# Performance work log

Hardware: AMD Instinct MI355X
Metric: run time of the kernel (lower is better)

## Reference

```python
import jax, jax.numpy as jnp
import numpy as np

B, T, NG, NH, DH = 16, 1024, 4, 1, 768
NS = 2  # states: (h, c)


def _lstm_layer(states0, Wx, R, b):
    """Fused LSTM scan for one layer.

    states0: [NS, B, NH, DH] initial (h, c)
    Wx:      [B, T, NG, NH, DH] precomputed input projections
    R:       [NG, NH, DH, DH] recurrent weights
    b:       [NG, NH, DH] biases
    returns: hs [T, NS, B, NH, DH] stacked (h, c) per step
    """
    h0, c0 = states0[0], states0[1]
    bb = b[:, None]  # [NG, 1, NH, DH] -> broadcasts over batch

    def step(carry, wx_t):
        h, c = carry  # [B, NH, DH]
        # gates: [NG, B, NH, DH]
        gates = wx_t + jnp.einsum('bhd,ghde->gbhe', h, R) + bb
        i = jax.nn.sigmoid(gates[0])
        f = jax.nn.sigmoid(gates[1])
        z = jnp.tanh(gates[2])
        o = jax.nn.sigmoid(gates[3])
        c_new = f * c + i * z
        h_new = o * jnp.tanh(c_new)
        return (h_new, c_new), jnp.stack([h_new, c_new])

    wx_tfirst = jnp.transpose(Wx, (1, 2, 0, 3, 4))  # [T, NG, B, NH, DH]
    _, hs = jax.lax.scan(step, (h0, c0), wx_tfirst)
    return hs  # [T, NS, B, NH, DH]


def setup_inputs() -> dict:
    key = jax.random.key(0)
    ks = jax.random.split(key, 6)
    s = 0.02
    return {
        'states': jnp.zeros((1, NS, B, NH, DH), jnp.float32),
        'Wx0': jax.random.normal(ks[0], (B, T, NG, NH, DH), jnp.float32) * s,
        'R0': jax.random.normal(ks[1], (NG, NH, DH, DH), jnp.float32) * s,
        'b0': jax.random.normal(ks[2], (NG, NH, DH), jnp.float32) * s,
        'Wx1': jax.random.normal(ks[3], (B, T, NG, NH, DH), jnp.float32) * s,
        'R1': jax.random.normal(ks[4], (NG, NH, DH, DH), jnp.float32) * s,
        'b1': jax.random.normal(ks[5], (NG, NH, DH), jnp.float32) * s,
    }


def reference(states, Wx0, R0, b0, Wx1, R1, b1):
    out = states  # [1, NS, B, NH, DH]
    h = None
    last_h = None
    for Wx, R, b in ((Wx0, R0, b0), (Wx1, R1, b1)):
        hs = _lstm_layer(out[0], Wx, R, b)  # [T, NS, B, NH, DH]
        h = hs
        last_h = hs[-1:]  # [1, NS, B, NH, DH]
        out = last_h  # last state of this layer is initial state of next
    return (h, last_h, out)
```

## Files before the change

kernel.cpp:

```cpp
#include <hip/hip_runtime.h>
#include <math.h>

#define NWG    48
#define TT     1024
#define BSZ    16
#define DHH    768
#define NGG    4
#define EC     16
#define LDR    776
#define GP     17
#define KS     192
#define FSTR   32

typedef __attribute__((ext_vector_type(8))) short bf16x8_t;
typedef __attribute__((ext_vector_type(4))) float f32x4_t;

__device__ __forceinline__ unsigned short f2bf(float f) {
  union { float f; unsigned int u; } v; v.f = f;
  return (unsigned short)((v.u + 0x7fffu + ((v.u >> 16) & 1u)) >> 16);
}

__device__ __forceinline__ bf16x8_t ld_h_frag(const unsigned short* p) {
  union { bf16x8_t v; unsigned long long q[2]; } u;
  u.q[0] = __hip_atomic_load((const unsigned long long*)p,       __ATOMIC_RELAXED, __HIP_MEMORY_SCOPE_AGENT);
  u.q[1] = __hip_atomic_load((const unsigned long long*)(p + 4), __ATOMIC_RELAXED, __HIP_MEMORY_SCOPE_AGENT);
  return u.v;
}

__global__ void lstm_init_ws(int* flags) {
  for (int i = threadIdx.x; i < NWG * FSTR; i += blockDim.x) flags[i] = 0;
}

__device__ __forceinline__ void grid_barrier(int* flags, int wg, int epoch, int lane, int wv) {
  __syncthreads();
  if (wv == 0) {
    if (lane == 0)
      __hip_atomic_store(flags + wg * FSTR, epoch, __ATOMIC_RELAXED, __HIP_MEMORY_SCOPE_AGENT);
    for (;;) {
      int v = (lane < NWG)
            ? __hip_atomic_load(flags + lane * FSTR, __ATOMIC_RELAXED, __HIP_MEMORY_SCOPE_AGENT)
            : epoch;
      if (__all(v >= epoch)) break;
      __builtin_amdgcn_s_sleep(1);
    }
  }
  __syncthreads();
}

__global__ __launch_bounds__(256, 1) void lstm_persistent(
    const float* __restrict__ states,
    const float* __restrict__ Wx0, const float* __restrict__ R0, const float* __restrict__ b0,
    const float* __restrict__ Wx1, const float* __restrict__ R1, const float* __restrict__ b1,
    float* __restrict__ out, int* __restrict__ flags, unsigned short* __restrict__ hbuf)
{
  extern __shared__ unsigned char smem[];
  unsigned short* r_lds    = (unsigned short*)smem;
  float*          part_lds = (float*)(r_lds + NGG * EC * LDR);
  float*          b_lds    = part_lds + 4 * NGG * BSZ * GP;

  const int tid  = threadIdx.x;
  const int lane = tid & 63;
  const int wv   = tid >> 6;
  const int bb   = tid >> 4;
  const int el   = tid & 15;
  const int wg   = blockIdx.x;
  const int e0   = wg * EC;
  const int m    = lane & 15;
  const int q    = lane >> 4;

  float creg = states[(BSZ + bb) * DHH + e0 + el];
  {
    unsigned hv = f2bf(states[bb * DHH + e0 + el]);
    unsigned pv = (unsigned)__shfl_xor((int)hv, 1, 64);
    if ((el & 1) == 0)
      __hip_atomic_store((unsigned*)(hbuf + bb * DHH + e0 + el), hv | (pv << 16),
                         __ATOMIC_RELAXED, __HIP_MEMORY_SCOPE_AGENT);
  }

  int epoch = 1;
  grid_barrier(flags, wg, epoch, lane, wv);

  for (int layer = 0; layer < 2; ++layer) {
    const float* Wx = layer ? Wx1 : Wx0;
    const float* Rm = layer ? R1  : R0;
    const float* bv = layer ? b1  : b0;

    for (int i = tid; i < NGG * DHH; i += 256) {
      const int g = i / DHH, d = i - g * DHH;
      const float* src = Rm + (g * DHH + d) * DHH + e0;
      #pragma unroll
      for (int n = 0; n < EC; ++n)
        r_lds[(g * EC + n) * LDR + d] = f2bf(src[n]);
    }
    if (tid < NGG * EC) b_lds[tid] = bv[(tid >> 4) * DHH + e0 + (tid & 15)];
    __syncthreads();

    for (int t = 0; t < TT; ++t) {
      const int gs = layer * TT + t;
      const unsigned short* __restrict__ hsrc = hbuf + (gs & 1) * (BSZ * DHH);
      unsigned short* __restrict__ hdst = hbuf + ((gs + 1) & 1) * (BSZ * DHH);

      const float* wxp = Wx + ((bb * TT + t) * NGG) * DHH + e0 + el;
      const float wxv0 = wxp[0];
      const float wxv1 = wxp[DHH];
      const float wxv2 = wxp[2 * DHH];
      const float wxv3 = wxp[3 * DHH];

      {
        const unsigned short* ha = hsrc + m * DHH + wv * KS + q * 8;
        const unsigned short* rb = r_lds + m * LDR + wv * KS + q * 8;
        f32x4_t ac0 = {0.f, 0.f, 0.f, 0.f};
        f32x4_t ac1 = ac0, ac2 = ac0, ac3 = ac0;
        #pragma unroll
        for (int kk = 0; kk < KS; kk += 32) {
          bf16x8_t av = ld_h_frag(ha + kk);
          ac0 = __builtin_amdgcn_mfma_f32_16x16x32_bf16(av, *(const bf16x8_t*)(rb + kk),               ac0, 0, 0, 0);
          ac1 = __builtin_amdgcn_mfma_f32_16x16x32_bf16(av, *(const bf16x8_t*)(rb + EC * LDR + kk),    ac1, 0, 0, 0);
          ac2 = __builtin_amdgcn_mfma_f32_16x16x32_bf16(av, *(const bf16x8_t*)(rb + 2 * EC * LDR + kk), ac2, 0, 0, 0);
          ac3 = __builtin_amdgcn_mfma_f32_16x16x32_bf16(av, *(const bf16x8_t*)(rb + 3 * EC * LDR + kk), ac3, 0, 0, 0);
        }
        #pragma unroll
        for (int r = 0; r < 4; ++r) {
          part_lds[((wv * NGG + 0) * BSZ + q * 4 + r) * GP + m] = ac0[r];
          part_lds[((wv * NGG + 1) * BSZ + q * 4 + r) * GP + m] = ac1[r];
          part_lds[((wv * NGG + 2) * BSZ + q * 4 + r) * GP + m] = ac2[r];
          part_lds[((wv * NGG + 3) * BSZ + q * 4 + r) * GP + m] = ac3[r];
        }
      }
      __syncthreads();

      {
        float gi = wxv0 + b_lds[0 * EC + el];
        float gf = wxv1 + b_lds[1 * EC + el];
        float gz = wxv2 + b_lds[2 * EC + el];
        float go = wxv3 + b_lds[3 * EC + el];
        #pragma unroll
        for (int w = 0; w < 4; ++w) {
          gi += part_lds[((w * NGG + 0) * BSZ + bb) * GP + el];
          gf += part_lds[((w * NGG + 1) * BSZ + bb) * GP + el];
          gz += part_lds[((w * NGG + 2) * BSZ + bb) * GP + el];
          go += part_lds[((w * NGG + 3) * BSZ + bb) * GP + el];
        }
        const float iv = 1.f / (1.f + __expf(-gi));
        const float fv = 1.f / (1.f + __expf(-gf));
        const float zv = tanhf(gz);
        const float ov = 1.f / (1.f + __expf(-go));
        const float cnew = fv * creg + iv * zv;
        const float hnew = ov * tanhf(cnew);
        creg = cnew;

        unsigned hv = f2bf(hnew);
        unsigned pv = (unsigned)__shfl_xor((int)hv, 1, 64);
        if ((el & 1) == 0)
          __hip_atomic_store((unsigned*)(hdst + bb * DHH + e0 + el), hv | (pv << 16),
                             __ATOMIC_RELAXED, __HIP_MEMORY_SCOPE_AGENT);

        if (layer == 1) {
          out[((t * 2 + 0) * BSZ + bb) * DHH + e0 + el] = hnew;
          out[((t * 2 + 1) * BSZ + bb) * DHH + e0 + el] = cnew;
          if (t == TT - 1) {
            const int HS = TT * 2 * BSZ * DHH;
            out[HS + (0 * BSZ + bb) * DHH + e0 + el] = hnew;
            out[HS + (1 * BSZ + bb) * DHH + e0 + el] = cnew;
            out[HS + 2 * BSZ * DHH + (0 * BSZ + bb) * DHH + e0 + el] = hnew;
            out[HS + 2 * BSZ * DHH + (1 * BSZ + bb) * DHH + e0 + el] = cnew;
          }
        }
      }

      if (gs != 2 * TT - 1) {
        ++epoch;
        grid_barrier(flags, wg, epoch, lane, wv);
      }
    }
  }
}

extern "C" void kernel_launch(void* const* d_in, const int* in_sizes, int n_in,
                              void* d_out, int out_size, void* d_ws, size_t ws_size,
                              hipStream_t stream) {
  const float* states = (const float*)d_in[0];
  const float* Wx0    = (const float*)d_in[1];
  const float* R0     = (const float*)d_in[2];
  const float* b0     = (const float*)d_in[3];
  const float* Wx1    = (const float*)d_in[4];
  const float* R1     = (const float*)d_in[5];
  const float* b1     = (const float*)d_in[6];
  float* out = (float*)d_out;

  int* flags = (int*)d_ws;
  unsigned short* hbuf = (unsigned short*)((char*)d_ws + 8192);

  const int smem_bytes = (NGG * EC * LDR) * 2 +
                         (4 * NGG * BSZ * GP + NGG * EC) * 4;

  static bool attr_set = false;
  if (!attr_set) {
    hipFuncSetAttribute((const void*)lstm_persistent,
                        hipFuncAttributeMaxDynamicSharedMemorySize, smem_bytes);
    attr_set = true;
  }

  lstm_init_ws<<<dim3(1), dim3(256), 0, stream>>>(flags);
  lstm_persistent<<<dim3(NWG), dim3(256), smem_bytes, stream>>>(
      states, Wx0, R0, b0, Wx1, R1, b1, out, flags, hbuf);
}
```

Baseline: 7.959 ms.

## Keep recurrent weights in registers, prefetch Wx, and make all waves poll the grid barrier

Recurrent weight fragments are loaded once per layer from LDS into registers, so the per-step MFMA loop no longer reads LDS. The next step's Wx values are prefetched one step ahead, and the h fragments are fetched with raw sc1 global loads issued together before a single wait. The grid barrier changes so that every wave polls the flags without sleeping, which removes one __syncthreads and the s_sleep delay. Sigmoid and tanh now use exp-based approximations and the biases live in registers. In exchange the kernel uses much more register space and relies on hand-written inline asm for memory ordering.

```diff
diff --git a/kernel.cpp b/kernel.cpp
--- a/kernel.cpp
+++ b/kernel.cpp
@@ -15,36 +15,44 @@
 typedef __attribute__((ext_vector_type(8))) short bf16x8_t;
 typedef __attribute__((ext_vector_type(4))) float f32x4_t;
 
+#define MF(a,b,c) __builtin_amdgcn_mfma_f32_16x16x32_bf16((a),(b),(c),0,0,0)
+
 __device__ __forceinline__ unsigned short f2bf(float f) {
   union { float f; unsigned int u; } v; v.f = f;
   return (unsigned short)((v.u + 0x7fffu + ((v.u >> 16) & 1u)) >> 16);
 }
-
-__device__ __forceinline__ bf16x8_t ld_h_frag(const unsigned short* p) {
-  union { bf16x8_t v; unsigned long long q[2]; } u;
-  u.q[0] = __hip_atomic_load((const unsigned long long*)p,       __ATOMIC_RELAXED, __HIP_MEMORY_SCOPE_AGENT);
-  u.q[1] = __hip_atomic_load((const unsigned long long*)(p + 4), __ATOMIC_RELAXED, __HIP_MEMORY_SCOPE_AGENT);
-  return u.v;
+__device__ __forceinline__ float sigm(float x)      { return 1.f / (1.f + __expf(-x)); }
+__device__ __forceinline__ float tanh_fast(float x) { return 1.f - 2.f / (__expf(2.f * x) + 1.f); }
+
+__device__ __forceinline__ void ldg_a16_sc(bf16x8_t& d, const unsigned short* p) {
+  asm volatile("global_load_dwordx4 %0, %1, off sc1" : "=v"(d) : "v"(p));
+}
+__device__ __forceinline__ void ldg_f32(float& d, const float* p) {
+  asm volatile("global_load_dword %0, %1, off" : "=v"(d) : "v"(p));
+}
+__device__ __forceinline__ void stg_u32_sc(unsigned* p, unsigned v) {
+  asm volatile("global_store_dword %0, %1, off sc1" :: "v"(p), "v"(v) : "memory");
+}
+__device__ __forceinline__ void wait_vm0() {
+  asm volatile("s_waitcnt vmcnt(0)" ::: "memory");
+}
+__device__ __forceinline__ void wait_lgkm_barrier() {
+  asm volatile("s_waitcnt lgkmcnt(0)\ns_barrier" ::: "memory");
+}
+__device__ __forceinline__ void wait_vm0_barrier() {
+  asm volatile("s_waitcnt vmcnt(0) lgkmcnt(0)\ns_barrier" ::: "memory");
 }
 
 __global__ void lstm_init_ws(int* flags) {
   for (int i = threadIdx.x; i < NWG * FSTR; i += blockDim.x) flags[i] = 0;
 }
 
-__device__ __forceinline__ void grid_barrier(int* flags, int wg, int epoch, int lane, int wv) {
-  __syncthreads();
-  if (wv == 0) {
-    if (lane == 0)
-      __hip_atomic_store(flags + wg * FSTR, epoch, __ATOMIC_RELAXED, __HIP_MEMORY_SCOPE_AGENT);
-    for (;;) {
-      int v = (lane < NWG)
-            ? __hip_atomic_load(flags + lane * FSTR, __ATOMIC_RELAXED, __HIP_MEMORY_SCOPE_AGENT)
-            : epoch;
-      if (__all(v >= epoch)) break;
-      __builtin_amdgcn_s_sleep(1);
-    }
-  }
-  __syncthreads();
+__device__ __forceinline__ void poll_flags(const int* fp, bool self_or_oob, int epoch) {
+  for (;;) {
+    int v = self_or_oob ? epoch
+                        : __hip_atomic_load(fp, __ATOMIC_RELAXED, __HIP_MEMORY_SCOPE_AGENT);
+    if (__all(v >= epoch)) break;
+  }
 }
 
 __global__ __launch_bounds__(256, 1) void lstm_persistent(
@@ -56,7 +64,6 @@
   extern __shared__ unsigned char smem[];
   unsigned short* r_lds    = (unsigned short*)smem;
   float*          part_lds = (float*)(r_lds + NGG * EC * LDR);
-  float*          b_lds    = part_lds + 4 * NGG * BSZ * GP;
 
   const int tid  = threadIdx.x;
   const int lane = tid & 63;
@@ -68,17 +75,33 @@
   const int m    = lane & 15;
   const int q    = lane >> 4;
 
+  const int aofs = m * DHH + wv * KS + q * 8;
+  const int hofs = bb * DHH + e0 + el;
+  const int* fp  = flags + (lane < NWG ? lane : 0) * FSTR;
+  const bool self_skip = (lane >= NWG) || (lane == wg);
+
   float creg = states[(BSZ + bb) * DHH + e0 + el];
   {
     unsigned hv = f2bf(states[bb * DHH + e0 + el]);
     unsigned pv = (unsigned)__shfl_xor((int)hv, 1, 64);
     if ((el & 1) == 0)
-      __hip_atomic_store((unsigned*)(hbuf + bb * DHH + e0 + el), hv | (pv << 16),
-                         __ATOMIC_RELAXED, __HIP_MEMORY_SCOPE_AGENT);
+      stg_u32_sc((unsigned*)(hbuf + hofs), hv | (pv << 16));
   }
 
   int epoch = 1;
-  grid_barrier(flags, wg, epoch, lane, wv);
+  wait_vm0_barrier();
+  if (tid == 0)
+    __hip_atomic_store(flags + wg * FSTR, epoch, __ATOMIC_RELAXED, __HIP_MEMORY_SCOPE_AGENT);
+  float pw0, pw1, pw2, pw3;
+  {
+    const float* wxp = Wx0 + ((bb * TT + 0) * NGG) * DHH + e0 + el;
+    ldg_f32(pw0, wxp); ldg_f32(pw1, wxp + DHH);
+    ldg_f32(pw2, wxp + 2 * DHH); ldg_f32(pw3, wxp + 3 * DHH);
+  }
+  poll_flags(fp, self_skip, epoch);
+  __builtin_amdgcn_sched_barrier(0);
+
+  int oofs = bb * DHH + e0 + el;
 
   for (int layer = 0; layer < 2; ++layer) {
     const float* Wx = layer ? Wx1 : Wx0;
@@ -92,48 +115,72 @@
       for (int n = 0; n < EC; ++n)
         r_lds[(g * EC + n) * LDR + d] = f2bf(src[n]);
     }
-    if (tid < NGG * EC) b_lds[tid] = bv[(tid >> 4) * DHH + e0 + (tid & 15)];
     __syncthreads();
+
+    bf16x8_t B00,B01,B02,B03,B04,B05, B10,B11,B12,B13,B14,B15,
+             B20,B21,B22,B23,B24,B25, B30,B31,B32,B33,B34,B35;
+    {
+      const unsigned short* rb = r_lds + m * LDR + wv * KS + q * 8;
+      B00 = *(const bf16x8_t*)(rb + 0*EC*LDR +   0); B01 = *(const bf16x8_t*)(rb + 0*EC*LDR +  32);
+      B02 = *(const bf16x8_t*)(rb + 0*EC*LDR +  64); B03 = *(const bf16x8_t*)(rb + 0*EC*LDR +  96);
+      B04 = *(const bf16x8_t*)(rb + 0*EC*LDR + 128); B05 = *(const bf16x8_t*)(rb + 0*EC*LDR + 160);
+      B10 = *(const bf16x8_t*)(rb + 1*EC*LDR +   0); B11 = *(const bf16x8_t*)(rb + 1*EC*LDR +  32);
+      B12 = *(const bf16x8_t*)(rb + 1*EC*LDR +  64); B13 = *(const bf16x8_t*)(rb + 1*EC*LDR +  96);
+      B14 = *(const bf16x8_t*)(rb + 1*EC*LDR + 128); B15 = *(const bf16x8_t*)(rb + 1*EC*LDR + 160);
+      B20 = *(const bf16x8_t*)(rb + 2*EC*LDR +   0); B21 = *(const bf16x8_t*)(rb + 2*EC*LDR +  32);
+      B22 = *(const bf16x8_t*)(rb + 2*EC*LDR +  64); B23 = *(const bf16x8_t*)(rb + 2*EC*LDR +  96);
+      B24 = *(const bf16x8_t*)(rb + 2*EC*LDR + 128); B25 = *(const bf16x8_t*)(rb + 2*EC*LDR + 160);
+      B30 = *(const bf16x8_t*)(rb + 3*EC*LDR +   0); B31 = *(const bf16x8_t*)(rb + 3*EC*LDR +  32);
+      B32 = *(const bf16x8_t*)(rb + 3*EC*LDR +  64); B33 = *(const bf16x8_t*)(rb + 3*EC*LDR +  96);
+      B34 = *(const bf16x8_t*)(rb + 3*EC*LDR + 128); B35 = *(const bf16x8_t*)(rb + 3*EC*LDR + 160);
+    }
+    const float bi_ = bv[0 * DHH + e0 + el];
+    const float bf_ = bv[1 * DHH + e0 + el];
+    const float bz_ = bv[2 * DHH + e0 + el];
+    const float bo_ = bv[3 * DHH + e0 + el];
 
     for (int t = 0; t < TT; ++t) {
       const int gs = layer * TT + t;
       const unsigned short* __restrict__ hsrc = hbuf + (gs & 1) * (BSZ * DHH);
       unsigned short* __restrict__ hdst = hbuf + ((gs + 1) & 1) * (BSZ * DHH);
 
-      const float* wxp = Wx + ((bb * TT + t) * NGG) * DHH + e0 + el;
-      const float wxv0 = wxp[0];
-      const float wxv1 = wxp[DHH];
-      const float wxv2 = wxp[2 * DHH];
-      const float wxv3 = wxp[3 * DHH];
-
+      const float qw0 = pw0, qw1 = pw1, qw2 = pw2, qw3 = pw3;
+
+      bf16x8_t av0, av1, av2, av3, av4, av5;
       {
-        const unsigned short* ha = hsrc + m * DHH + wv * KS + q * 8;
-        const unsigned short* rb = r_lds + m * LDR + wv * KS + q * 8;
-        f32x4_t ac0 = {0.f, 0.f, 0.f, 0.f};
-        f32x4_t ac1 = ac0, ac2 = ac0, ac3 = ac0;
-        #pragma unroll
-        for (int kk = 0; kk < KS; kk += 32) {
-          bf16x8_t av = ld_h_frag(ha + kk);
-          ac0 = __builtin_amdgcn_mfma_f32_16x16x32_bf16(av, *(const bf16x8_t*)(rb + kk),               ac0, 0, 0, 0);
-          ac1 = __builtin_amdgcn_mfma_f32_16x16x32_bf16(av, *(const bf16x8_t*)(rb + EC * LDR + kk),    ac1, 0, 0, 0);
-          ac2 = __builtin_amdgcn_mfma_f32_16x16x32_bf16(av, *(const bf16x8_t*)(rb + 2 * EC * LDR + kk), ac2, 0, 0, 0);
-          ac3 = __builtin_amdgcn_mfma_f32_16x16x32_bf16(av, *(const bf16x8_t*)(rb + 3 * EC * LDR + kk), ac3, 0, 0, 0);
-        }
-        #pragma unroll
-        for (int r = 0; r < 4; ++r) {
-          part_lds[((wv * NGG + 0) * BSZ + q * 4 + r) * GP + m] = ac0[r];
-          part_lds[((wv * NGG + 1) * BSZ + q * 4 + r) * GP + m] = ac1[r];
-          part_lds[((wv * NGG + 2) * BSZ + q * 4 + r) * GP + m] = ac2[r];
-          part_lds[((wv * NGG + 3) * BSZ + q * 4 + r) * GP + m] = ac3[r];
-        }
-      }
-      __syncthreads();
+        const unsigned short* ha = hsrc + aofs;
+        ldg_a16_sc(av0, ha +   0); ldg_a16_sc(av1, ha +  32);
+        ldg_a16_sc(av2, ha +  64); ldg_a16_sc(av3, ha +  96);
+        ldg_a16_sc(av4, ha + 128); ldg_a16_sc(av5, ha + 160);
+      }
+      if (gs + 1 < 2 * TT) {
+        const int g2 = gs + 1, l2 = g2 >> 10, t2 = g2 & (TT - 1);
+        const float* wxp = (l2 ? Wx1 : Wx0) + ((bb * TT + t2) * NGG) * DHH + e0 + el;
+        ldg_f32(pw0, wxp); ldg_f32(pw1, wxp + DHH);
+        ldg_f32(pw2, wxp + 2 * DHH); ldg_f32(pw3, wxp + 3 * DHH);
+      }
+      wait_vm0();
+      __builtin_amdgcn_sched_barrier(0);
+
+      f32x4_t ac0 = {0.f,0.f,0.f,0.f}, ac1 = ac0, ac2 = ac0, ac3 = ac0;
+      ac0 = MF(av0,B00,ac0); ac1 = MF(av0,B10,ac1); ac2 = MF(av0,B20,ac2); ac3 = MF(av0,B30,ac3);
+      ac0 = MF(av1,B01,ac0); ac1 = MF(av1,B11,ac1); ac2 = MF(av1,B21,ac2); ac3 = MF(av1,B31,ac3);
+      ac0 = MF(av2,B02,ac0); ac1 = MF(av2,B12,ac1); ac2 = MF(av2,B22,ac2); ac3 = MF(av2,B32,ac3);
+      ac0 = MF(av3,B03,ac0); ac1 = MF(av3,B13,ac1); ac2 = MF(av3,B23,ac2); ac3 = MF(av3,B33,ac3);
+      ac0 = MF(av4,B04,ac0); ac1 = MF(av4,B14,ac1); ac2 = MF(av4,B24,ac2); ac3 = MF(av4,B34,ac3);
+      ac0 = MF(av5,B05,ac0); ac1 = MF(av5,B15,ac1); ac2 = MF(av5,B25,ac2); ac3 = MF(av5,B35,ac3);
+
+      #pragma unroll
+      for (int r = 0; r < 4; ++r) {
+        part_lds[((wv * NGG + 0) * BSZ + q * 4 + r) * GP + m] = ac0[r];
+        part_lds[((wv * NGG + 1) * BSZ + q * 4 + r) * GP + m] = ac1[r];
+        part_lds[((wv * NGG + 2) * BSZ + q * 4 + r) * GP + m] = ac2[r];
+        part_lds[((wv * NGG + 3) * BSZ + q * 4 + r) * GP + m] = ac3[r];
+      }
+      wait_lgkm_barrier();
 
       {
-        float gi = wxv0 + b_lds[0 * EC + el];
-        float gf = wxv1 + b_lds[1 * EC + el];
-        float gz = wxv2 + b_lds[2 * EC + el];
-        float go = wxv3 + b_lds[3 * EC + el];
+        float gi = qw0 + bi_, gf = qw1 + bf_, gz = qw2 + bz_, go = qw3 + bo_;
         #pragma unroll
         for (int w = 0; w < 4; ++w) {
           gi += part_lds[((w * NGG + 0) * BSZ + bb) * GP + el];
@@ -141,36 +188,37 @@
           gz += part_lds[((w * NGG + 2) * BSZ + bb) * GP + el];
           go += part_lds[((w * NGG + 3) * BSZ + bb) * GP + el];
         }
-        const float iv = 1.f / (1.f + __expf(-gi));
-        const float fv = 1.f / (1.f + __expf(-gf));
-        const float zv = tanhf(gz);
-        const float ov = 1.f / (1.f + __expf(-go));
+        const float iv = sigm(gi), fv = sigm(gf), zv = tanh_fast(gz), ov = sigm(go);
         const float cnew = fv * creg + iv * zv;
-        const float hnew = ov * tanhf(cnew);
+        const float hnew = ov * tanh_fast(cnew);
         creg = cnew;
 
         unsigned hv = f2bf(hnew);
         unsigned pv = (unsigned)__shfl_xor((int)hv, 1, 64);
         if ((el & 1) == 0)
-          __hip_atomic_store((unsigned*)(hdst + bb * DHH + e0 + el), hv | (pv << 16),
-                             __ATOMIC_RELAXED, __HIP_MEMORY_SCOPE_AGENT);
+          stg_u32_sc((unsigned*)(hdst + hofs), hv | (pv << 16));
 
         if (layer == 1) {
-          out[((t * 2 + 0) * BSZ + bb) * DHH + e0 + el] = hnew;
-          out[((t * 2 + 1) * BSZ + bb) * DHH + e0 + el] = cnew;
+          out[oofs] = hnew;
+          out[oofs + BSZ * DHH] = cnew;
           if (t == TT - 1) {
             const int HS = TT * 2 * BSZ * DHH;
-            out[HS + (0 * BSZ + bb) * DHH + e0 + el] = hnew;
-            out[HS + (1 * BSZ + bb) * DHH + e0 + el] = cnew;
-            out[HS + 2 * BSZ * DHH + (0 * BSZ + bb) * DHH + e0 + el] = hnew;
-            out[HS + 2 * BSZ * DHH + (1 * BSZ + bb) * DHH + e0 + el] = cnew;
+            out[HS + bb * DHH + e0 + el] = hnew;
+            out[HS + BSZ * DHH + bb * DHH + e0 + el] = cnew;
+            out[HS + 2 * BSZ * DHH + bb * DHH + e0 + el] = hnew;
+            out[HS + 3 * BSZ * DHH + bb * DHH + e0 + el] = cnew;
           }
+          oofs += 2 * BSZ * DHH;
         }
       }
 
       if (gs != 2 * TT - 1) {
         ++epoch;
-        grid_barrier(flags, wg, epoch, lane, wv);
+        wait_vm0_barrier();
+        if (tid == 0)
+          __hip_atomic_store(flags + wg * FSTR, epoch, __ATOMIC_RELAXED, __HIP_MEMORY_SCOPE_AGENT);
+        poll_flags(fp, self_skip, epoch);
+        __builtin_amdgcn_sched_barrier(0);
       }
     }
   }
@@ -191,8 +239,7 @@
   int* flags = (int*)d_ws;
   unsigned short* hbuf = (unsigned short*)((char*)d_ws + 8192);
 
-  const int smem_bytes = (NGG * EC * LDR) * 2 +
-                         (4 * NGG * BSZ * GP + NGG * EC) * 4;
+  const int smem_bytes = (NGG * EC * LDR) * 2 + (4 * NGG * BSZ * GP) * 4;
 
   static bool attr_set = false;
   if (!attr_set) {
```

Result: faster. 7.112 ms (-10.6%).
